# Performance work log

Hardware: AMD Instinct MI355X
Metric: run time of the kernel (lower is better)

Reference implementation:

```python
import jax, jax.numpy as jnp
import numpy as np

K = 17
PAD = K // 2
THRESHOLD = 55.0
TEMPERATURE = 20.0


def _normalize_0_100(x, eps=1e-8):
    x_min = jnp.min(x)
    x_max = jnp.max(x)
    return 100.0 * (x - x_min) / jnp.maximum(x_max - x_min, eps)


def setup_inputs() -> dict:
    key = jax.random.key(0)
    k1, k2, k3, k4 = jax.random.split(key, 4)
    H_total, W_total = 512, 512
    Fdim, Odim = 100, 180
    f_print1 = jax.random.uniform(k1, (H_total, W_total), dtype=jnp.float32)
    freq_ind = jax.random.randint(k2, (H_total, W_total), 0, Fdim)
    orient_ind = jax.random.randint(k3, (H_total, W_total), 0, Odim)
    filterbank = jax.random.normal(k4, (Fdim, Odim, K, K), dtype=jnp.float32)
    return {
        "f_print1": f_print1,
        "freq_ind": freq_ind,
        "orient_ind": orient_ind,
        "filterbank": filterbank,
        "H": 480,
        "W": 480,
        "margin": 32,
    }


def reference(f_print1, freq_ind, orient_ind, filterbank, H, W, margin):
    Fdim, Odim, K1, K2 = filterbank.shape
    H_total, W_total = f_print1.shape
    # im2col: zero-padded sliding KxK windows, row-major over the kernel window
    # (matches torch F.unfold ordering for a single channel)
    x_pad = jnp.pad(f_print1, PAD)
    ih = jnp.arange(H_total)[:, None] + jnp.arange(K)[None, :]  # (H_total, K)
    iw = jnp.arange(W_total)[:, None] + jnp.arange(K)[None, :]  # (W_total, K)
    patches = x_pad[ih[:, None, :, None], iw[None, :, None, :]]  # (H,W,K,K)

    # per-pixel kernel gather (indices are 1-based in the source, clamped)
    f0 = jnp.clip(freq_ind - 1, 0, Fdim - 1)
    o0 = jnp.clip(orient_ind - 1, 0, Odim - 1)
    idx = f0 * Odim + o0  # (H,W)
    kernels = filterbank.reshape(Fdim * Odim, K, K)[idx]  # (H,W,K,K)

    # spatially-varying convolution: per-pixel multiply + reduce
    y = jnp.einsum('hwkl,hwkl->hw', patches, kernels)

    out = _normalize_0_100(y)
    out = 100.0 * jax.nn.sigmoid(TEMPERATURE * (out / 100.0 - THRESHOLD / 100.0))
    out = _normalize_0_100(out)
    return out
```

## Files before the change

### kernel.cpp

```cpp
#include <hip/hip_runtime.h>
#include <math.h>

#define FDIM  100
#define ODIM  180
#define HTOT  512
#define WTOT  512
#define TILE  32
#define REG   48
#define LDSW  49
#define NSLICE 8
#define SLICE_SZ 2250
#define NTILE 256
#define NBLK  (NTILE * NSLICE)
#define TEMPERATURE 20.0f
#define THRESHOLD   55.0f

__global__ __launch_bounds__(256) void filter_sliced(
    const float* __restrict__ x,
    const int*   __restrict__ freq,
    const int*   __restrict__ orient,
    const float* __restrict__ fb,
    float*       __restrict__ y,
    float2*      __restrict__ partial)
{
    __shared__ float tile[REG][LDSW];
    __shared__ int   sidx[TILE * TILE];
    __shared__ unsigned short sel[TILE * TILE];
    __shared__ unsigned int nsel;

    const int gid   = blockIdx.x;
    const int slice = gid & (NSLICE - 1);
    const int t     = gid >> 3;
    const int bx    = t & 15, by = t >> 4;
    const int tid   = threadIdx.x;

    if (tid == 0) nsel = 0;
    __syncthreads();

    const int lo = slice * SLICE_SZ;
    #pragma unroll
    for (int k = 0; k < 4; ++k) {
        const int p  = tid + k * 256;
        const int pr = p >> 5, pc = p & 31;
        const int pid = (by * TILE + pr) * WTOT + bx * TILE + pc;
        int f0 = freq[pid] - 1;
        int o0 = orient[pid] - 1;
        f0 = f0 < 0 ? 0 : (f0 > FDIM - 1 ? FDIM - 1 : f0);
        o0 = o0 < 0 ? 0 : (o0 > ODIM - 1 ? ODIM - 1 : o0);
        const int idx = f0 * ODIM + o0;
        sidx[p] = idx;
        if (idx >= lo && idx < lo + SLICE_SZ) {
            unsigned int s = atomicAdd(&nsel, 1u);
            sel[s] = (unsigned short)p;
        }
    }

    const int h0 = by * TILE - 8;
    const int w0 = bx * TILE - 8;
    for (int i = tid; i < REG * REG; i += 256) {
        const int r = i / REG, c = i - r * REG;
        const int gh = h0 + r, gw = w0 + c;
        float v = 0.f;
        if (gh >= 0 && gh < HTOT && gw >= 0 && gw < WTOT)
            v = x[gh * WTOT + gw];
        tile[r][c] = v;
    }
    __syncthreads();

    const unsigned int m = nsel;
    const int l  = tid & 15;
    const int qw = tid >> 4;

    int offs[18];
    #pragma unroll
    for (int j = 0; j < 18; ++j) {
        const int e = j * 16 + l;
        offs[j] = (e / 17) * LDSW + (e % 17);
    }

    float mn = 3.4e38f, mx = -3.4e38f;

    for (unsigned int s = qw; s < m; s += 16) {
        const int tp  = sel[s];
        const int ppy = tp >> 5, ppx = tp & 31;
        const float* __restrict__ kf = fb + (size_t)sidx[tp] * 289;

        float kv[18];
        #pragma unroll
        for (int j = 0; j < 18; ++j) kv[j] = kf[j * 16 + l];
        const float kt = kf[288];

        const float* __restrict__ base = &tile[ppy][ppx];
        float a0 = 0.f, a1 = 0.f, a2 = 0.f, a3 = 0.f;
        #pragma unroll
        for (int j = 0; j < 16; j += 4) {
            a0 = fmaf(kv[j    ], base[offs[j    ]], a0);
            a1 = fmaf(kv[j + 1], base[offs[j + 1]], a1);
            a2 = fmaf(kv[j + 2], base[offs[j + 2]], a2);
            a3 = fmaf(kv[j + 3], base[offs[j + 3]], a3);
        }
        a0 = fmaf(kv[16], base[offs[16]], a0);
        a1 = fmaf(kv[17], base[offs[17]], a1);
        float acc = (a0 + a1) + (a2 + a3);
        if (l == 0) acc = fmaf(kt, base[16 * LDSW + 16], acc);

        #pragma unroll
        for (int off = 8; off; off >>= 1)
            acc += __shfl_xor(acc, off, 64);

        if (l == 0)
            y[(by * TILE + ppy) * WTOT + bx * TILE + ppx] = acc;
        mn = fminf(mn, acc);
        mx = fmaxf(mx, acc);
    }

    #pragma unroll
    for (int off = 32; off > 0; off >>= 1) {
        mn = fminf(mn, __shfl_down(mn, off, 64));
        mx = fmaxf(mx, __shfl_down(mx, off, 64));
    }
    __shared__ float smn[4], smx[4];
    const int wid = tid >> 6, lane = tid & 63;
    if (lane == 0) { smn[wid] = mn; smx[wid] = mx; }
    __syncthreads();
    if (tid == 0) {
        float bmn = smn[0], bmx = smx[0];
        #pragma unroll
        for (int i = 1; i < 4; ++i) {
            bmn = fminf(bmn, smn[i]);
            bmx = fmaxf(bmx, smx[i]);
        }
        partial[gid] = make_float2(bmn, bmx);
    }
}

__global__ __launch_bounds__(256) void reduce_mm(
    const float2* __restrict__ partial,
    float* __restrict__ mmf)
{
    const int tid = threadIdx.x;
    float mn = 3.4e38f, mx = -3.4e38f;
    for (int i = tid; i < NBLK; i += 256) {
        const float2 p = partial[i];
        mn = fminf(mn, p.x);
        mx = fmaxf(mx, p.y);
    }
    #pragma unroll
    for (int off = 32; off > 0; off >>= 1) {
        mn = fminf(mn, __shfl_down(mn, off, 64));
        mx = fmaxf(mx, __shfl_down(mx, off, 64));
    }
    __shared__ float smn[4], smx[4];
    const int wid = tid >> 6, lane = tid & 63;
    if (lane == 0) { smn[wid] = mn; smx[wid] = mx; }
    __syncthreads();
    if (tid == 0) {
        float bmn = smn[0], bmx = smx[0];
        #pragma unroll
        for (int i = 1; i < 4; ++i) {
            bmn = fminf(bmn, smn[i]);
            bmx = fmaxf(bmx, smx[i]);
        }
        mmf[0] = bmn;
        mmf[1] = bmx;
    }
}

__global__ __launch_bounds__(256) void filter_final(
    float* __restrict__ y,
    const float* __restrict__ mmf)
{
    const int i = blockIdx.x * 256 + threadIdx.x;
    const float ymin = mmf[0];
    const float ymax = mmf[1];
    const float rng  = fmaxf(ymax - ymin, 1e-8f);

    const float v  = y[i];
    const float o1 = 100.f * (v - ymin) / rng;
    const float s  = 100.f / (1.f + expf(-(TEMPERATURE * (o1 * 0.01f - THRESHOLD * 0.01f))));

    const float smin = 100.f / (1.f + expf( 11.f));
    const float smax = 100.f / (1.f + expf(-9.f));
    const float srng = fmaxf(smax - smin, 1e-8f);

    y[i] = 100.f * (s - smin) / srng;
}

extern "C" void kernel_launch(void* const* d_in, const int* in_sizes, int n_in,
                              void* d_out, int out_size, void* d_ws, size_t ws_size,
                              hipStream_t stream) {
    const float* x      = (const float*)d_in[0];
    const int*   freq   = (const int*)d_in[1];
    const int*   orient = (const int*)d_in[2];
    const float* fb     = (const float*)d_in[3];
    float*       out    = (float*)d_out;
    float2*      partial = (float2*)d_ws;
    float*       mmf    = (float*)((char*)d_ws + 16384);

    filter_sliced<<<dim3(NBLK), 256, 0, stream>>>(x, freq, orient, fb, out, partial);

    reduce_mm<<<1, 256, 0, stream>>>(partial, mmf);

    filter_final<<<(HTOT * WTOT) / 256, 256, 0, stream>>>(out, mmf);
}
```

Measured before the change: 34.87 us.

## Repack filterbank into padded 320-stride layout for vectorized float4 loads

Adds a pre-pass kernel that copies the 289-element filters into a zero-padded 320-float stride, interleaved so each lane can fetch its coefficients with five 16-byte loads instead of eighteen scalar loads plus a tail load. The tail special case for the last coefficient is removed because the padding contributes zeros. The cost is an extra kernel that reads the whole 20 MB filterbank and writes about 23 MB on every call, while the main kernel only touches the filters that pixels actually select.

```diff
diff --git a/kernel.cpp b/kernel.cpp
--- a/kernel.cpp
+++ b/kernel.cpp
@@ -3,6 +3,7 @@
 
 #define FDIM  100
 #define ODIM  180
+#define NFILT (FDIM * ODIM)
 #define HTOT  512
 #define WTOT  512
 #define TILE  32
@@ -12,14 +13,39 @@
 #define SLICE_SZ 2250
 #define NTILE 256
 #define NBLK  (NTILE * NSLICE)
+#define RSTRIDE 320
 #define TEMPERATURE 20.0f
 #define THRESHOLD   55.0f
+
+typedef float f32x4 __attribute__((ext_vector_type(4)));
+
+#define WS_PARTIAL 23040000
+#define WS_MMF     (WS_PARTIAL + 16384)
+
+__global__ __launch_bounds__(256) void repack_fb(
+    const float* __restrict__ fb,
+    float*       __restrict__ rfb)
+{
+    const int q = blockIdx.x * 256 + threadIdx.x;
+    if (q >= NFILT * (RSTRIDE / 4)) return;
+    const int f = q / (RSTRIDE / 4);
+    const int r = q - f * (RSTRIDE / 4);
+    const int J = r >> 4, l = r & 15;
+    const float* __restrict__ src = fb + (size_t)f * 289;
+    f32x4 v;
+    #pragma unroll
+    for (int i = 0; i < 4; ++i) {
+        const int e = 64 * J + 16 * i + l;
+        v[i] = (e <= 288) ? src[e] : 0.f;
+    }
+    reinterpret_cast<f32x4*>(rfb)[q] = v;
+}
 
 __global__ __launch_bounds__(256) void filter_sliced(
     const float* __restrict__ x,
     const int*   __restrict__ freq,
     const int*   __restrict__ orient,
-    const float* __restrict__ fb,
+    const float* __restrict__ rfb,
     float*       __restrict__ y,
     float2*      __restrict__ partial)
 {
@@ -71,10 +97,11 @@
     const int l  = tid & 15;
     const int qw = tid >> 4;
 
-    int offs[18];
-    #pragma unroll
-    for (int j = 0; j < 18; ++j) {
-        const int e = j * 16 + l;
+    int offs[20];
+    #pragma unroll
+    for (int j = 0; j < 20; ++j) {
+        int e = j * 16 + l;
+        e = e > 288 ? 288 : e;
         offs[j] = (e / 17) * LDSW + (e % 17);
     }
 
@@ -83,26 +110,23 @@
     for (unsigned int s = qw; s < m; s += 16) {
         const int tp  = sel[s];
         const int ppy = tp >> 5, ppx = tp & 31;
-        const float* __restrict__ kf = fb + (size_t)sidx[tp] * 289;
-
-        float kv[18];
-        #pragma unroll
-        for (int j = 0; j < 18; ++j) kv[j] = kf[j * 16 + l];
-        const float kt = kf[288];
+        const float* __restrict__ kf = rfb + (size_t)sidx[tp] * RSTRIDE;
+
+        f32x4 kq[5];
+        #pragma unroll
+        for (int J = 0; J < 5; ++J)
+            kq[J] = *reinterpret_cast<const f32x4*>(kf + J * 64 + 4 * l);
 
         const float* __restrict__ base = &tile[ppy][ppx];
         float a0 = 0.f, a1 = 0.f, a2 = 0.f, a3 = 0.f;
         #pragma unroll
-        for (int j = 0; j < 16; j += 4) {
-            a0 = fmaf(kv[j    ], base[offs[j    ]], a0);
-            a1 = fmaf(kv[j + 1], base[offs[j + 1]], a1);
-            a2 = fmaf(kv[j + 2], base[offs[j + 2]], a2);
-            a3 = fmaf(kv[j + 3], base[offs[j + 3]], a3);
-        }
-        a0 = fmaf(kv[16], base[offs[16]], a0);
-        a1 = fmaf(kv[17], base[offs[17]], a1);
+        for (int J = 0; J < 5; ++J) {
+            a0 = fmaf(kq[J].x, base[offs[4 * J + 0]], a0);
+            a1 = fmaf(kq[J].y, base[offs[4 * J + 1]], a1);
+            a2 = fmaf(kq[J].z, base[offs[4 * J + 2]], a2);
+            a3 = fmaf(kq[J].w, base[offs[4 * J + 3]], a3);
+        }
         float acc = (a0 + a1) + (a2 + a3);
-        if (l == 0) acc = fmaf(kt, base[16 * LDSW + 16], acc);
 
         #pragma unroll
         for (int off = 8; off; off >>= 1)
@@ -194,10 +218,14 @@
     const int*   orient = (const int*)d_in[2];
     const float* fb     = (const float*)d_in[3];
     float*       out    = (float*)d_out;
-    float2*      partial = (float2*)d_ws;
-    float*       mmf    = (float*)((char*)d_ws + 16384);
-
-    filter_sliced<<<dim3(NBLK), 256, 0, stream>>>(x, freq, orient, fb, out, partial);
+    float*       rfb    = (float*)d_ws;
+    float2*      partial = (float2*)((char*)d_ws + WS_PARTIAL);
+    float*       mmf    = (float*)((char*)d_ws + WS_MMF);
+
+    const int nq = NFILT * (RSTRIDE / 4);
+    repack_fb<<<(nq + 255) / 256, 256, 0, stream>>>(fb, rfb);
+
+    filter_sliced<<<dim3(NBLK), 256, 0, stream>>>(x, freq, orient, rfb, out, partial);
 
     reduce_mm<<<1, 256, 0, stream>>>(partial, mmf);
 
```

Measured after the change: 48.31 us. +38.5%, slower.

## Prefetch next filter kernel, warp-aggregate selection atomics, fuse min/max reduce into final pass

Applied to the files above, without the earlier changes.

The filter loop now loads the next selected pixel's 289-tap filter into registers while the current one is being computed, so global-load latency overlaps with the FMA and shuffle work. Pixel selection uses a ballot plus one atomicAdd per wavefront instead of one atomic per pixel. The separate single-block min/max reduction kernel is removed: each block of the final normalization kernel re-reduces the 2048 partials itself and then processes four pixels per thread with vector loads and stores. This drops one kernel launch at the cost of redundant partial reads in every block and higher register use from the prefetch buffers.

```diff
diff --git a/kernel.cpp b/kernel.cpp
--- a/kernel.cpp
+++ b/kernel.cpp
@@ -15,6 +15,8 @@
 #define TEMPERATURE 20.0f
 #define THRESHOLD   55.0f
 
+typedef float f32x4 __attribute__((ext_vector_type(4)));
+
 __global__ __launch_bounds__(256) void filter_sliced(
     const float* __restrict__ x,
     const int*   __restrict__ freq,
@@ -33,6 +35,7 @@
     const int t     = gid >> 3;
     const int bx    = t & 15, by = t >> 4;
     const int tid   = threadIdx.x;
+    const int lane  = tid & 63;
 
     if (tid == 0) nsel = 0;
     __syncthreads();
@@ -49,9 +52,14 @@
         o0 = o0 < 0 ? 0 : (o0 > ODIM - 1 ? ODIM - 1 : o0);
         const int idx = f0 * ODIM + o0;
         sidx[p] = idx;
-        if (idx >= lo && idx < lo + SLICE_SZ) {
-            unsigned int s = atomicAdd(&nsel, 1u);
-            sel[s] = (unsigned short)p;
+        const bool want = (idx >= lo && idx < lo + SLICE_SZ);
+        const unsigned long long mask = __ballot(want);
+        unsigned int base = 0;
+        if (lane == 0) base = atomicAdd(&nsel, (unsigned int)__popcll(mask));
+        base = __shfl(base, 0, 64);
+        if (want) {
+            const int pos = __popcll(mask & ((1ULL << lane) - 1ULL));
+            sel[base + pos] = (unsigned short)p;
         }
     }
 
@@ -80,16 +88,29 @@
 
     float mn = 3.4e38f, mx = -3.4e38f;
 
+    float kv[19];
+    int   cur_tp = 0;
+    if (qw < (int)m) {
+        cur_tp = sel[qw];
+        const float* __restrict__ kf = fb + (size_t)sidx[cur_tp] * 289;
+        #pragma unroll
+        for (int j = 0; j < 18; ++j) kv[j] = kf[j * 16 + l];
+        kv[18] = kf[288];
+    }
+
     for (unsigned int s = qw; s < m; s += 16) {
-        const int tp  = sel[s];
-        const int ppy = tp >> 5, ppx = tp & 31;
-        const float* __restrict__ kf = fb + (size_t)sidx[tp] * 289;
-
-        float kv[18];
-        #pragma unroll
-        for (int j = 0; j < 18; ++j) kv[j] = kf[j * 16 + l];
-        const float kt = kf[288];
-
+        const unsigned int sn = s + 16;
+        float kn[19];
+        int   nxt_tp = 0;
+        if (sn < m) {
+            nxt_tp = sel[sn];
+            const float* __restrict__ kf = fb + (size_t)sidx[nxt_tp] * 289;
+            #pragma unroll
+            for (int j = 0; j < 18; ++j) kn[j] = kf[j * 16 + l];
+            kn[18] = kf[288];
+        }
+
+        const int ppy = cur_tp >> 5, ppx = cur_tp & 31;
         const float* __restrict__ base = &tile[ppy][ppx];
         float a0 = 0.f, a1 = 0.f, a2 = 0.f, a3 = 0.f;
         #pragma unroll
@@ -102,7 +123,7 @@
         a0 = fmaf(kv[16], base[offs[16]], a0);
         a1 = fmaf(kv[17], base[offs[17]], a1);
         float acc = (a0 + a1) + (a2 + a3);
-        if (l == 0) acc = fmaf(kt, base[16 * LDSW + 16], acc);
+        if (l == 0) acc = fmaf(kv[18], base[16 * LDSW + 16], acc);
 
         #pragma unroll
         for (int off = 8; off; off >>= 1)
@@ -112,6 +133,12 @@
             y[(by * TILE + ppy) * WTOT + bx * TILE + ppx] = acc;
         mn = fminf(mn, acc);
         mx = fmaxf(mx, acc);
+
+        if (sn < m) {
+            cur_tp = nxt_tp;
+            #pragma unroll
+            for (int j = 0; j < 19; ++j) kv[j] = kn[j];
+        }
     }
 
     #pragma unroll
@@ -120,7 +147,7 @@
         mx = fmaxf(mx, __shfl_down(mx, off, 64));
     }
     __shared__ float smn[4], smx[4];
-    const int wid = tid >> 6, lane = tid & 63;
+    const int wid = tid >> 6;
     if (lane == 0) { smn[wid] = mn; smx[wid] = mx; }
     __syncthreads();
     if (tid == 0) {
@@ -134,9 +161,9 @@
     }
 }
 
-__global__ __launch_bounds__(256) void reduce_mm(
-    const float2* __restrict__ partial,
-    float* __restrict__ mmf)
+__global__ __launch_bounds__(256) void filter_final(
+    float* __restrict__ y,
+    const float2* __restrict__ partial)
 {
     const int tid = threadIdx.x;
     float mn = 3.4e38f, mx = -3.4e38f;
@@ -154,6 +181,7 @@
     const int wid = tid >> 6, lane = tid & 63;
     if (lane == 0) { smn[wid] = mn; smx[wid] = mx; }
     __syncthreads();
+    __shared__ float sfin[2];
     if (tid == 0) {
         float bmn = smn[0], bmx = smx[0];
         #pragma unroll
@@ -161,29 +189,25 @@
             bmn = fminf(bmn, smn[i]);
             bmx = fmaxf(bmx, smx[i]);
         }
-        mmf[0] = bmn;
-        mmf[1] = bmx;
-    }
-}
-
-__global__ __launch_bounds__(256) void filter_final(
-    float* __restrict__ y,
-    const float* __restrict__ mmf)
-{
-    const int i = blockIdx.x * 256 + threadIdx.x;
-    const float ymin = mmf[0];
-    const float ymax = mmf[1];
-    const float rng  = fmaxf(ymax - ymin, 1e-8f);
-
-    const float v  = y[i];
-    const float o1 = 100.f * (v - ymin) / rng;
-    const float s  = 100.f / (1.f + expf(-(TEMPERATURE * (o1 * 0.01f - THRESHOLD * 0.01f))));
-
+        sfin[0] = bmn; sfin[1] = bmx;
+    }
+    __syncthreads();
+
+    const float ymin = sfin[0];
+    const float rng  = fmaxf(sfin[1] - ymin, 1e-8f);
     const float smin = 100.f / (1.f + expf( 11.f));
     const float smax = 100.f / (1.f + expf(-9.f));
     const float srng = fmaxf(smax - smin, 1e-8f);
 
-    y[i] = 100.f * (s - smin) / srng;
+    const int base = blockIdx.x * 1024 + tid * 4;
+    f32x4 v = *reinterpret_cast<const f32x4*>(&y[base]);
+    #pragma unroll
+    for (int i = 0; i < 4; ++i) {
+        const float o1 = 100.f * (v[i] - ymin) / rng;
+        const float s  = 100.f / (1.f + expf(-(TEMPERATURE * (o1 * 0.01f - THRESHOLD * 0.01f))));
+        v[i] = 100.f * (s - smin) / srng;
+    }
+    *reinterpret_cast<f32x4*>(&y[base]) = v;
 }
 
 extern "C" void kernel_launch(void* const* d_in, const int* in_sizes, int n_in,
@@ -195,11 +219,8 @@
     const float* fb     = (const float*)d_in[3];
     float*       out    = (float*)d_out;
     float2*      partial = (float2*)d_ws;
-    float*       mmf    = (float*)((char*)d_ws + 16384);
 
     filter_sliced<<<dim3(NBLK), 256, 0, stream>>>(x, freq, orient, fb, out, partial);
 
-    reduce_mm<<<1, 256, 0, stream>>>(partial, mmf);
-
-    filter_final<<<(HTOT * WTOT) / 256, 256, 0, stream>>>(out, mmf);
+    filter_final<<<(HTOT * WTOT) / 1024, 256, 0, stream>>>(out, partial);
 }
```

After: 42.79 us. +22.7%, slower.
